# Kernel optimization log

Measured on AMD Instinct MI355X. Metric: run time of the kernel, lower is better.

## Reference

```python
import jax, jax.numpy as jnp
import numpy as np

N = 8192
NFEAT = 512
NHID = 256
NCLASS = 128


def setup_inputs() -> dict:
    key = jax.random.key(0)
    k1, k2, k3, k4 = jax.random.split(key, 4)
    feature_s = jax.random.normal(k1, (N, NFEAT), dtype=jnp.float32)
    feature_t = jax.random.normal(k2, (N, NFEAT), dtype=jnp.float32)
    # nn.Linear(in, out, bias=False) weight has shape [out, in]
    w1 = jax.random.normal(k3, (NHID, NFEAT), dtype=jnp.float32) * (1.0 / np.sqrt(NFEAT))
    w2 = jax.random.normal(k4, (NCLASS, NHID), dtype=jnp.float32) * (1.0 / np.sqrt(NHID))
    return {"feature_s": feature_s, "feature_t": feature_t, "w1": w1, "w2": w2}


def reference(feature_s, feature_t, w1, w2):
    # adj = softmax(feature_s @ feature_t^T) over rows (dim=1)
    adj = jax.nn.softmax(feature_s @ feature_t.T, axis=1)  # [N, N]
    # GCN layer 1: linear(adj @ x) with x = feature_s
    x1 = (adj @ feature_s) @ w1.T  # [N, NHID]
    # GCN layer 2
    x2 = (adj @ x1) @ w2.T  # [N, NCLASS]
    return (x1, x2)
```

## Files before the change

### kernel.cpp

```cpp
#include <hip/hip_runtime.h>
#include <stdint.h>


typedef unsigned short u16;
typedef short bf16x8 __attribute__((ext_vector_type(8)));
typedef _Float16 f16x8 __attribute__((ext_vector_type(8)));
typedef float f32x4 __attribute__((ext_vector_type(4)));

#define EPI_STOREB 0
#define EPI_PARTH  1

__device__ __forceinline__ u16 f2bf(float f) {
  unsigned u = __float_as_uint(f);
  u += 0x7fffu + ((u >> 16) & 1u);
  return (u16)(u >> 16);
}
__device__ __forceinline__ u16 f2h(float f) {
  union { _Float16 h; u16 u; } cv; cv.h = (_Float16)f; return cv.u;
}
__device__ __forceinline__ float h2f(u16 u) {
  union { u16 u; _Float16 h; } cv; cv.u = u; return (float)cv.h;
}
__device__ __forceinline__ int swz8(int r) { return (r ^ (r >> 3)) & 7; }
__device__ __forceinline__ int swz16(int r) { return (r ^ (r >> 4)) & 15; }

__device__ __forceinline__ void async16(const void* g, void* lds) {
  __builtin_amdgcn_global_load_lds(
      (const __attribute__((address_space(1))) unsigned int*)g,
      (__attribute__((address_space(3))) unsigned int*)lds, 16, 0, 0);
}

__global__ __launch_bounds__(256) void conv_probe(
    const float* __restrict__ Fs, const float* __restrict__ Ft,
    const float* __restrict__ W1, const float* __restrict__ W2,
    u16* __restrict__ Fsf, u16* __restrict__ Ftf,
    u16* __restrict__ W1f, u16* __restrict__ W2h,
    int* __restrict__ rmap, int* __restrict__ cmap) {
  const int bx = blockIdx.x, tid = threadIdx.x;
  if (bx < 4176) {
    const float* src; u16* dst; size_t i; bool tobf = false;
    if (bx < 2048)      { src = Fs; dst = Fsf; i = ((size_t)bx * 256 + tid) * 8; }
    else if (bx < 4096) { src = Ft; dst = Ftf; i = ((size_t)(bx - 2048) * 256 + tid) * 8; }
    else if (bx < 4160) { src = W1; dst = W1f; i = ((size_t)(bx - 4096) * 256 + tid) * 8; }
    else                { src = W2; dst = W2h; i = ((size_t)(bx - 4160) * 256 + tid) * 8; tobf = true; }
    const float4 a = *(const float4*)(src + i);
    const float4 b = *(const float4*)(src + i + 4);
    bf16x8 o;
    if (tobf) {
      o[0] = (short)f2bf(a.x); o[1] = (short)f2bf(a.y); o[2] = (short)f2bf(a.z); o[3] = (short)f2bf(a.w);
      o[4] = (short)f2bf(b.x); o[5] = (short)f2bf(b.y); o[6] = (short)f2bf(b.z); o[7] = (short)f2bf(b.w);
    } else {
      o[0] = (short)f2h(a.x); o[1] = (short)f2h(a.y); o[2] = (short)f2h(a.z); o[3] = (short)f2h(a.w);
      o[4] = (short)f2h(b.x); o[5] = (short)f2h(b.y); o[6] = (short)f2h(b.z); o[7] = (short)f2h(b.w);
    }
    *(bf16x8*)(dst + i) = o;
    return;
  }
  if (tid >= 64) return;
  const int lane = tid & 63;
  const int t = lane & 15, quad = lane >> 4;
  bf16x8 avt, av1;
  const u16 bt = f2bf((float)t), b1 = 0x3f80;
#pragma unroll
  for (int j = 0; j < 8; ++j) { ((u16*)&avt)[j] = bt; ((u16*)&av1)[j] = b1; }
  f32x4 z = {0.f, 0.f, 0.f, 0.f};
  f32x4 r1 = __builtin_amdgcn_mfma_f32_16x16x32_bf16(avt, av1, z, 0, 0, 0);
  f32x4 r2 = __builtin_amdgcn_mfma_f32_16x16x32_bf16(av1, avt, z, 0, 0, 0);
#pragma unroll
  for (int e = 0; e < 4; ++e) {
    int r = (int)(r1[e] * 0.03125f + 0.5f);
    int c = (int)(r2[e] * 0.03125f + 0.5f);
    if (r < 0 || r > 15) r = quad * 4 + e;
    if (c < 0 || c > 15) c = t;
    rmap[lane * 4 + e] = r;
    cmap[lane * 4 + e] = c;
  }
}

__global__ __launch_bounds__(512) void gemm_pexp_f16_256(
    const u16* __restrict__ A, const u16* __restrict__ B, int K, int N,
    u16* __restrict__ P, float* __restrict__ rsp,
    const int* __restrict__ rmap, const int* __restrict__ cmap) {
  __shared__ __align__(16) u16 lA[256 * 64];
  __shared__ __align__(16) u16 lB[128 * 64];
  __shared__ float lrs[256][2];

  const int tid = threadIdx.x;
  const int wave = tid >> 6, lane = tid & 63;
  const int quad = lane >> 4, t = lane & 15;
  const int bm = blockIdx.y * 256, bn = blockIdx.x * 128;
  const int wm = (wave & 3) * 64, wn = (wave >> 2) * 64;

  f32x4 acc[4][4];
#pragma unroll
  for (int i = 0; i < 4; ++i)
#pragma unroll
    for (int j = 0; j < 4; ++j) acc[i][j] = (f32x4){0.f, 0.f, 0.f, 0.f};

  const int srow = tid >> 3, schk = tid & 7;
  const u16* pA[4]; const u16* pB[2];
#pragma unroll
  for (int j = 0; j < 4; ++j) {
    const int r = j * 64 + srow;
    pA[j] = A + (size_t)(bm + r) * K + (schk ^ swz8(r)) * 8;
  }
#pragma unroll
  for (int j = 0; j < 2; ++j) {
    const int r = j * 64 + srow;
    pB[j] = B + (size_t)(bn + r) * K + (schk ^ swz8(r)) * 8;
  }

  int aoffx[4], boffx[4];
#pragma unroll
  for (int i = 0; i < 4; ++i) {
    const int rm = wm + i * 16 + t;
    aoffx[i] = rm * 128 + (swz8(rm) << 4);
    const int rn = wn + i * 16 + t;
    boffx[i] = rn * 128 + (swz8(rn) << 4);
  }
  const int sq0 = quad << 4, sq1 = (quad << 4) | 64;

  for (int k0 = 0; k0 < K; k0 += 64) {
#pragma unroll
    for (int j = 0; j < 4; ++j) {
      async16(pA[j], (char*)lA + j * 8192 + wave * 1024);
      pA[j] += 64;
    }
#pragma unroll
    for (int j = 0; j < 2; ++j) {
      async16(pB[j], (char*)lB + j * 8192 + wave * 1024);
      pB[j] += 64;
    }
    __syncthreads();
#pragma unroll
    for (int s = 0; s < 2; ++s) {
      const int sq = s ? sq1 : sq0;
      f16x8 av[4], bv[4];
#pragma unroll
      for (int i = 0; i < 4; ++i) {
        av[i] = *(const f16x8*)((const char*)lA + (aoffx[i] ^ sq));
        bv[i] = *(const f16x8*)((const char*)lB + (boffx[i] ^ sq));
      }
#pragma unroll
      for (int mi = 0; mi < 4; ++mi)
#pragma unroll
        for (int ni = 0; ni < 4; ++ni)
          acc[mi][ni] = __builtin_amdgcn_mfma_f32_16x16x32_f16(av[mi], bv[ni], acc[mi][ni], 0, 0, 0);
    }
    __syncthreads();
  }

  int rl[4], cl[4];
#pragma unroll
  for (int e = 0; e < 4; ++e) {
    rl[e] = rmap[lane * 4 + e];
    cl[e] = cmap[lane * 4 + e];
  }
#pragma unroll
  for (int mi = 0; mi < 4; ++mi)
#pragma unroll
    for (int e = 0; e < 4; ++e) {
      const int rloc = wm + mi * 16 + rl[e];
      const int row = bm + rloc;
      float s = 0.f;
#pragma unroll
      for (int ni = 0; ni < 4; ++ni) {
        float p = __expf(acc[mi][ni][e] - 100.0f);
        s += p;
        P[(size_t)row * N + (bn + wn + ni * 16 + cl[e])] = f2bf(p);
      }
      s += __shfl_xor(s, 1, 64);
      s += __shfl_xor(s, 2, 64);
      s += __shfl_xor(s, 4, 64);
      s += __shfl_xor(s, 8, 64);
      if (t == 0) lrs[rloc][wave >> 2] = s;
    }
  __syncthreads();
  if (tid < 256)
    rsp[(size_t)blockIdx.x * 8192 + bm + tid] = lrs[tid][0] + lrs[tid][1];
}

__global__ __launch_bounds__(256) void finalize_invl(
    const float* __restrict__ rsp, float* __restrict__ invl) {
  const int row = blockIdx.x * 256 + threadIdx.x;
  float s = 0.f;
#pragma unroll 8
  for (int b = 0; b < 64; ++b) s += rsp[(size_t)b * 8192 + row];
  invl[row] = 1.0f / s;
}

template <int EPI, int F16>
__global__ __launch_bounds__(256) void gemm_nt(
    const u16* __restrict__ A, const u16* __restrict__ B, int K, int Kc, int N,
    u16* __restrict__ outp, const float* __restrict__ invl,
    const int* __restrict__ rmap, const int* __restrict__ cmap) {
  __shared__ __align__(16) u16 lA[128 * 64];
  __shared__ __align__(16) u16 lB[128 * 64];

  const int tid = threadIdx.x;
  const int wave = tid >> 6, lane = tid & 63;
  const int quad = lane >> 4, t = lane & 15;
  const int bm = blockIdx.y * 128, bn = blockIdx.x * 128;
  const int wm = (wave & 1) * 64, wn = (wave >> 1) * 64;
  const int koff = blockIdx.z * Kc;

  f32x4 acc[4][4];
#pragma unroll
  for (int i = 0; i < 4; ++i)
#pragma unroll
    for (int j = 0; j < 4; ++j) acc[i][j] = (f32x4){0.f, 0.f, 0.f, 0.f};

  const int srow = tid >> 3, schk = tid & 7;
  const u16* pA[4]; const u16* pB[4];
#pragma unroll
  for (int j = 0; j < 4; ++j) {
    const int r = j * 32 + srow;
    const int c = schk ^ swz8(r);
    pA[j] = A + (size_t)(bm + r) * K + koff + c * 8;
    pB[j] = B + (size_t)(bn + r) * K + koff + c * 8;
  }

  int aoffx[4], boffx[4];
#pragma unroll
  for (int i = 0; i < 4; ++i) {
    const int rm = wm + i * 16 + t;
    aoffx[i] = rm * 128 + (swz8(rm) << 4);
    const int rn = wn + i * 16 + t;
    boffx[i] = rn * 128 + (swz8(rn) << 4);
  }
  const int sq0 = quad << 4, sq1 = (quad << 4) | 64;

  for (int k0 = 0; k0 < Kc; k0 += 64) {
#pragma unroll
    for (int j = 0; j < 4; ++j) {
      async16(pA[j], (char*)lA + j * 4096 + wave * 1024);
      async16(pB[j], (char*)lB + j * 4096 + wave * 1024);
      pA[j] += 64; pB[j] += 64;
    }
    __syncthreads();
#pragma unroll
    for (int s = 0; s < 2; ++s) {
      const int sq = s ? sq1 : sq0;
      bf16x8 av[4], bv[4];
#pragma unroll
      for (int i = 0; i < 4; ++i) {
        av[i] = *(const bf16x8*)((const char*)lA + (aoffx[i] ^ sq));
        bv[i] = *(const bf16x8*)((const char*)lB + (boffx[i] ^ sq));
      }
#pragma unroll
      for (int mi = 0; mi < 4; ++mi)
#pragma unroll
        for (int ni = 0; ni < 4; ++ni) {
          if constexpr (F16)
            acc[mi][ni] = __builtin_amdgcn_mfma_f32_16x16x32_f16(
                __builtin_bit_cast(f16x8, av[mi]), __builtin_bit_cast(f16x8, bv[ni]),
                acc[mi][ni], 0, 0, 0);
          else
            acc[mi][ni] = __builtin_amdgcn_mfma_f32_16x16x32_bf16(av[mi], bv[ni], acc[mi][ni], 0, 0, 0);
        }
    }
    __syncthreads();
  }

  int rl[4], cl[4];
#pragma unroll
  for (int e = 0; e < 4; ++e) {
    rl[e] = rmap[lane * 4 + e];
    cl[e] = cmap[lane * 4 + e];
  }
  const size_t zoff = (size_t)blockIdx.z * ((size_t)gridDim.y * 128) * N;
#pragma unroll
  for (int mi = 0; mi < 4; ++mi)
#pragma unroll
    for (int e = 0; e < 4; ++e) {
      const int row = bm + wm + mi * 16 + rl[e];
      const float sc = (EPI == EPI_PARTH) ? invl[row] : 1.0f;
#pragma unroll
      for (int ni = 0; ni < 4; ++ni) {
        const size_t idx = (size_t)row * N + (bn + wn + ni * 16 + cl[e]);
        if (EPI == EPI_PARTH) outp[zoff + idx] = f2h(acc[mi][ni][e] * sc);
        else                  outp[idx] = f2bf(acc[mi][ni][e]);
      }
    }
}

__global__ __launch_bounds__(256) void gemm_nt128(
    const u16* __restrict__ A, const u16* __restrict__ B, int K, int Kc, int N,
    u16* __restrict__ outp, const float* __restrict__ invl,
    const int* __restrict__ rmap, const int* __restrict__ cmap) {
  __shared__ __align__(16) u16 lA[128 * 128];
  __shared__ __align__(16) u16 lB[128 * 128];

  const int tid = threadIdx.x;
  const int wave = tid >> 6, lane = tid & 63;
  const int quad = lane >> 4, t = lane & 15;
  const int bm = blockIdx.y * 128, bn = blockIdx.x * 128;
  const int wm = (wave & 1) * 64, wn = (wave >> 1) * 64;
  const int koff = blockIdx.z * Kc;

  f32x4 acc[4][4];
#pragma unroll
  for (int i = 0; i < 4; ++i)
#pragma unroll
    for (int j = 0; j < 4; ++j) acc[i][j] = (f32x4){0.f, 0.f, 0.f, 0.f};

  const int srow = tid >> 4, schk = tid & 15;
  const u16* pA[8]; const u16* pB[8];
#pragma unroll
  for (int j = 0; j < 8; ++j) {
    const int r = j * 16 + srow;
    const int c = schk ^ swz16(r);
    pA[j] = A + (size_t)(bm + r) * K + koff + c * 8;
    pB[j] = B + (size_t)(bn + r) * K + koff + c * 8;
  }

  int aoffx[4], boffx[4];
#pragma unroll
  for (int i = 0; i < 4; ++i) {
    const int rm = wm + i * 16 + t;
    aoffx[i] = rm * 256 + (swz16(rm) << 4);
    const int rn = wn + i * 16 + t;
    boffx[i] = rn * 256 + (swz16(rn) << 4);
  }

  for (int k0 = 0; k0 < Kc; k0 += 128) {
#pragma unroll
    for (int j = 0; j < 8; ++j) {
      async16(pA[j], (char*)lA + j * 4096 + tid * 16);
      async16(pB[j], (char*)lB + j * 4096 + tid * 16);
      pA[j] += 128; pB[j] += 128;
    }
    __syncthreads();
#pragma unroll
    for (int s = 0; s < 4; ++s) {
      const int sq = (s << 6) | (quad << 4);
      bf16x8 av[4], bv[4];
#pragma unroll
      for (int i = 0; i < 4; ++i) {
        av[i] = *(const bf16x8*)((const char*)lA + (aoffx[i] ^ sq));
        bv[i] = *(const bf16x8*)((const char*)lB + (boffx[i] ^ sq));
      }
#pragma unroll
      for (int mi = 0; mi < 4; ++mi)
#pragma unroll
        for (int ni = 0; ni < 4; ++ni)
          acc[mi][ni] = __builtin_amdgcn_mfma_f32_16x16x32_bf16(av[mi], bv[ni], acc[mi][ni], 0, 0, 0);
    }
    __syncthreads();
  }

  int rl[4], cl[4];
#pragma unroll
  for (int e = 0; e < 4; ++e) {
    rl[e] = rmap[lane * 4 + e];
    cl[e] = cmap[lane * 4 + e];
  }
  const size_t zoff = (size_t)blockIdx.z * ((size_t)gridDim.y * 128) * N;
#pragma unroll
  for (int mi = 0; mi < 4; ++mi)
#pragma unroll
    for (int e = 0; e < 4; ++e) {
      const int row = bm + wm + mi * 16 + rl[e];
      const float sc = invl[row];
#pragma unroll
      for (int ni = 0; ni < 4; ++ni) {
        const size_t idx = (size_t)row * N + (bn + wn + ni * 16 + cl[e]);
        outp[zoff + idx] = f2h(acc[mi][ni][e] * sc);
      }
    }
}

__global__ __launch_bounds__(512) void gemm_ntw128(
    const u16* __restrict__ A, const u16* __restrict__ B, int K, int Kc, int N,
    u16* __restrict__ outp, const float* __restrict__ invl,
    const int* __restrict__ rmap, const int* __restrict__ cmap) {
  __shared__ __align__(16) u16 lA[128 * 128];
  __shared__ __align__(16) u16 lB[256 * 128];

  const int tid = threadIdx.x;
  const int wave = tid >> 6, lane = tid & 63;
  const int quad = lane >> 4, t = lane & 15;
  const int bm = blockIdx.y * 128, bn = blockIdx.x * 256;
  const int wm = (wave >> 2) * 64, wn = (wave & 3) * 64;
  const int koff = blockIdx.z * Kc;

  f32x4 acc[4][4];
#pragma unroll
  for (int i = 0; i < 4; ++i)
#pragma unroll
    for (int j = 0; j < 4; ++j) acc[i][j] = (f32x4){0.f, 0.f, 0.f, 0.f};

  const int srow = tid >> 4, schk = tid & 15;
  const u16* pA[4]; const u16* pB[8];
#pragma unroll
  for (int j = 0; j < 4; ++j) {
    const int r = j * 32 + srow;
    pA[j] = A + (size_t)(bm + r) * K + koff + (schk ^ swz16(r)) * 8;
  }
#pragma unroll
  for (int j = 0; j < 8; ++j) {
    const int r = j * 32 + srow;
    pB[j] = B + (size_t)(bn + r) * K + koff + (schk ^ swz16(r)) * 8;
  }

  int aoffx[4], boffx[4];
#pragma unroll
  for (int i = 0; i < 4; ++i) {
    const int rm = wm + i * 16 + t;
    aoffx[i] = rm * 256 + (swz16(rm) << 4);
    const int rn = wn + i * 16 + t;
    boffx[i] = rn * 256 + (swz16(rn) << 4);
  }

  for (int k0 = 0; k0 < Kc; k0 += 128) {
#pragma unroll
    for (int j = 0; j < 4; ++j) {
      async16(pA[j], (char*)lA + j * 8192 + tid * 16);
      pA[j] += 128;
    }
#pragma unroll
    for (int j = 0; j < 8; ++j) {
      async16(pB[j], (char*)lB + j * 8192 + tid * 16);
      pB[j] += 128;
    }
    __syncthreads();
#pragma unroll
    for (int s = 0; s < 4; ++s) {
      const int sq = (s << 6) | (quad << 4);
      bf16x8 av[4], bv[4];
#pragma unroll
      for (int i = 0; i < 4; ++i) {
        av[i] = *(const bf16x8*)((const char*)lA + (aoffx[i] ^ sq));
        bv[i] = *(const bf16x8*)((const char*)lB + (boffx[i] ^ sq));
      }
#pragma unroll
      for (int mi = 0; mi < 4; ++mi)
#pragma unroll
        for (int ni = 0; ni < 4; ++ni)
          acc[mi][ni] = __builtin_amdgcn_mfma_f32_16x16x32_bf16(av[mi], bv[ni], acc[mi][ni], 0, 0, 0);
    }
    __syncthreads();
  }

  int rl[4], cl[4];
#pragma unroll
  for (int e = 0; e < 4; ++e) {
    rl[e] = rmap[lane * 4 + e];
    cl[e] = cmap[lane * 4 + e];
  }
  const size_t zoff = (size_t)blockIdx.z * ((size_t)gridDim.y * 128) * N;
#pragma unroll
  for (int mi = 0; mi < 4; ++mi)
#pragma unroll
    for (int e = 0; e < 4; ++e) {
      const int row = bm + wm + mi * 16 + rl[e];
      const float sc = invl[row];
#pragma unroll
      for (int ni = 0; ni < 4; ++ni) {
        const size_t idx = (size_t)row * N + (bn + wn + ni * 16 + cl[e]);
        outp[zoff + idx] = f2h(acc[mi][ni][e] * sc);
      }
    }
}

__global__ __launch_bounds__(256) void combine1(
    const u16* __restrict__ pp, const float* __restrict__ invl,
    float* __restrict__ x1f, u16* __restrict__ x1h) {
  const size_t i = ((size_t)blockIdx.x * 256 + threadIdx.x) * 8;
  const bf16x8 p0 = *(const bf16x8*)(pp + i);
  const bf16x8 p1 = *(const bf16x8*)(pp + 2097152 + i);
  const bf16x8 p2 = *(const bf16x8*)(pp + 4194304 + i);
  const bf16x8 p3 = *(const bf16x8*)(pp + 6291456 + i);
  float4 o0, o1;
  bf16x8 oh;
#pragma unroll
  for (int j = 0; j < 8; ++j) {
    const float v = h2f((u16)p0[j]) + h2f((u16)p1[j]) + h2f((u16)p2[j]) + h2f((u16)p3[j]);
    if (j < 4) ((float*)&o0)[j] = v; else ((float*)&o1)[j - 4] = v;
    oh[j] = (short)f2bf(v);
  }
  *(float4*)(x1f + i) = o0;
  *(float4*)(x1f + i + 4) = o1;
  *(bf16x8*)(x1h + i) = oh;
}

__global__ __launch_bounds__(256) void combine2(
    const u16* __restrict__ pp, const float* __restrict__ invl,
    float* __restrict__ x2f) {
  const size_t i = ((size_t)blockIdx.x * 256 + threadIdx.x) * 8;
  float v[8] = {0.f, 0.f, 0.f, 0.f, 0.f, 0.f, 0.f, 0.f};
#pragma unroll
  for (int z = 0; z < 8; ++z) {
    const bf16x8 p = *(const bf16x8*)(pp + (size_t)z * 1048576 + i);
#pragma unroll
    for (int j = 0; j < 8; ++j) v[j] += h2f((u16)p[j]);
  }
  float4 o0, o1;
#pragma unroll
  for (int j = 0; j < 4; ++j) { ((float*)&o0)[j] = v[j]; ((float*)&o1)[j] = v[j + 4]; }
  *(float4*)(x2f + i) = o0;
  *(float4*)(x2f + i + 4) = o1;
}

extern "C" void kernel_launch(void* const* d_in, const int* in_sizes, int n_in,
                              void* d_out, int out_size, void* d_ws, size_t ws_size,
                              hipStream_t stream) {
  const float* Fs = (const float*)d_in[0];
  const float* Ft = (const float*)d_in[1];
  const float* W1 = (const float*)d_in[2];
  const float* W2 = (const float*)d_in[3];

  char* ws = (char*)d_ws;
  u16*   P    = (u16*)(ws);
  u16*   Fsf  = (u16*)(ws + 134217728);
  u16*   Ftf  = (u16*)(ws + 142606336);
  u16*   pp   = (u16*)(ws + 134217728);
  float* rsp  = (float*)(ws + 150994944);
  u16*   Y1T  = (u16*)(ws + 153092096);
  u16*   x1h  = (u16*)(ws + 157286400);
  u16*   Y2T  = (u16*)(ws + 161480704);
  float* invl = (float*)(ws + 163577856);
  int*   rmap = (int*)  (ws + 163610624);
  int*   cmap = (int*)  (ws + 163611648);
  u16*   W1f  = (u16*)(ws + 163612672);
  u16*   W2h  = (u16*)(ws + 163874816);

  float* x1f = (float*)d_out;
  float* x2f = (float*)d_out + 2097152;

  dim3 blk(256);
  conv_probe<<<4177, blk, 0, stream>>>(Fs, Ft, W1, W2, Fsf, Ftf, W1f, W2h, rmap, cmap);
  gemm_pexp_f16_256<<<dim3(64, 32), dim3(512), 0, stream>>>(
      Fsf, Ftf, 512, 8192, P, rsp, rmap, cmap);
  finalize_invl<<<32, blk, 0, stream>>>(rsp, invl);
  gemm_nt<EPI_STOREB, 1><<<dim3(64, 2), blk, 0, stream>>>(
      W1f, Fsf, 512, 512, 8192, Y1T, nullptr, rmap, cmap);
  gemm_ntw128<<<dim3(1, 64, 4), dim3(512), 0, stream>>>(
      P, Y1T, 8192, 2048, 256, pp, invl, rmap, cmap);
  combine1<<<1024, blk, 0, stream>>>(pp, invl, x1f, x1h);
  gemm_nt<EPI_STOREB, 0><<<dim3(64, 1), blk, 0, stream>>>(
      W2h, x1h, 256, 256, 8192, Y2T, nullptr, rmap, cmap);
  gemm_nt128<<<dim3(1, 64, 8), blk, 0, stream>>>(
      P, Y2T, 8192, 1024, 128, pp, invl, rmap, cmap);
  combine2<<<512, blk, 0, stream>>>(pp, invl, x2f);
}
```

Measured before the change: 276.8 us.

## Fuse invl finalize into GEMMs and combine1 with second-layer Y2T GEMM

Removes the finalize_invl kernel by having each split-K GEMM block sum its 128 rows' partial row-sums into shared memory. Merges combine1 and the small W2 GEMM into one kernel that reduces the split-K partials, writes x1 in fp32, and keeps the bf16 x1 tile in LDS to compute Y2T directly. This removes three launches and the x1h round trip through global memory. The cost is that every split-K block now repeats the 64-way row-sum reduction, and the fused kernel runs only 64 blocks.

New measurement: 279.3 us. Within noise of the previous version (+0.9%).

```diff
diff --git a/kernel.cpp b/kernel.cpp
--- a/kernel.cpp
+++ b/kernel.cpp
@@ -180,15 +180,6 @@
     rsp[(size_t)blockIdx.x * 8192 + bm + tid] = lrs[tid][0] + lrs[tid][1];
 }
 
-__global__ __launch_bounds__(256) void finalize_invl(
-    const float* __restrict__ rsp, float* __restrict__ invl) {
-  const int row = blockIdx.x * 256 + threadIdx.x;
-  float s = 0.f;
-#pragma unroll 8
-  for (int b = 0; b < 64; ++b) s += rsp[(size_t)b * 8192 + row];
-  invl[row] = 1.0f / s;
-}
-
 template <int EPI, int F16>
 __global__ __launch_bounds__(256) void gemm_nt(
     const u16* __restrict__ A, const u16* __restrict__ B, int K, int Kc, int N,
@@ -286,10 +277,11 @@
 
 __global__ __launch_bounds__(256) void gemm_nt128(
     const u16* __restrict__ A, const u16* __restrict__ B, int K, int Kc, int N,
-    u16* __restrict__ outp, const float* __restrict__ invl,
+    u16* __restrict__ outp, const float* __restrict__ rsp,
     const int* __restrict__ rmap, const int* __restrict__ cmap) {
   __shared__ __align__(16) u16 lA[128 * 128];
   __shared__ __align__(16) u16 lB[128 * 128];
+  __shared__ float linvl[128];
 
   const int tid = threadIdx.x;
   const int wave = tid >> 6, lane = tid & 63;
@@ -298,6 +290,14 @@
   const int wm = (wave & 1) * 64, wn = (wave >> 1) * 64;
   const int koff = blockIdx.z * Kc;
 
+  if (tid < 128) {
+    const int row = bm + tid;
+    float s = 0.f;
+#pragma unroll 8
+    for (int b = 0; b < 64; ++b) s += rsp[(size_t)b * 8192 + row];
+    linvl[tid] = 1.0f / s;
+  }
+
   f32x4 acc[4][4];
 #pragma unroll
   for (int i = 0; i < 4; ++i)
@@ -360,8 +360,9 @@
   for (int mi = 0; mi < 4; ++mi)
 #pragma unroll
     for (int e = 0; e < 4; ++e) {
-      const int row = bm + wm + mi * 16 + rl[e];
-      const float sc = invl[row];
+      const int rloc = wm + mi * 16 + rl[e];
+      const int row = bm + rloc;
+      const float sc = linvl[rloc];
 #pragma unroll
       for (int ni = 0; ni < 4; ++ni) {
         const size_t idx = (size_t)row * N + (bn + wn + ni * 16 + cl[e]);
@@ -372,10 +373,11 @@
 
 __global__ __launch_bounds__(512) void gemm_ntw128(
     const u16* __restrict__ A, const u16* __restrict__ B, int K, int Kc, int N,
-    u16* __restrict__ outp, const float* __restrict__ invl,
+    u16* __restrict__ outp, const float* __restrict__ rsp,
     const int* __restrict__ rmap, const int* __restrict__ cmap) {
   __shared__ __align__(16) u16 lA[128 * 128];
   __shared__ __align__(16) u16 lB[256 * 128];
+  __shared__ float linvl[128];
 
   const int tid = threadIdx.x;
   const int wave = tid >> 6, lane = tid & 63;
@@ -384,6 +386,14 @@
   const int wm = (wave >> 2) * 64, wn = (wave & 3) * 64;
   const int koff = blockIdx.z * Kc;
 
+  if (tid < 128) {
+    const int row = bm + tid;
+    float s = 0.f;
+#pragma unroll 8
+    for (int b = 0; b < 64; ++b) s += rsp[(size_t)b * 8192 + row];
+    linvl[tid] = 1.0f / s;
+  }
+
   f32x4 acc[4][4];
 #pragma unroll
   for (int i = 0; i < 4; ++i)
@@ -453,8 +463,9 @@
   for (int mi = 0; mi < 4; ++mi)
 #pragma unroll
     for (int e = 0; e < 4; ++e) {
-      const int row = bm + wm + mi * 16 + rl[e];
-      const float sc = invl[row];
+      const int rloc = wm + mi * 16 + rl[e];
+      const int row = bm + rloc;
+      const float sc = linvl[rloc];
 #pragma unroll
       for (int ni = 0; ni < 4; ++ni) {
         const size_t idx = (size_t)row * N + (bn + wn + ni * 16 + cl[e]);
@@ -463,25 +474,111 @@
     }
 }
 
-__global__ __launch_bounds__(256) void combine1(
-    const u16* __restrict__ pp, const float* __restrict__ invl,
-    float* __restrict__ x1f, u16* __restrict__ x1h) {
-  const size_t i = ((size_t)blockIdx.x * 256 + threadIdx.x) * 8;
-  const bf16x8 p0 = *(const bf16x8*)(pp + i);
-  const bf16x8 p1 = *(const bf16x8*)(pp + 2097152 + i);
-  const bf16x8 p2 = *(const bf16x8*)(pp + 4194304 + i);
-  const bf16x8 p3 = *(const bf16x8*)(pp + 6291456 + i);
-  float4 o0, o1;
-  bf16x8 oh;
-#pragma unroll
-  for (int j = 0; j < 8; ++j) {
-    const float v = h2f((u16)p0[j]) + h2f((u16)p1[j]) + h2f((u16)p2[j]) + h2f((u16)p3[j]);
-    if (j < 4) ((float*)&o0)[j] = v; else ((float*)&o1)[j - 4] = v;
-    oh[j] = (short)f2bf(v);
-  }
-  *(float4*)(x1f + i) = o0;
-  *(float4*)(x1f + i + 4) = o1;
-  *(bf16x8*)(x1h + i) = oh;
+__global__ __launch_bounds__(256) void c1gy2(
+    const u16* __restrict__ pp, const u16* __restrict__ W2h,
+    float* __restrict__ x1f, u16* __restrict__ Y2T,
+    const int* __restrict__ rmap, const int* __restrict__ cmap) {
+  __shared__ __align__(16) u16 x1l[4][128][64];
+  __shared__ __align__(16) u16 lA[128 * 64];
+
+  const int tid = threadIdx.x;
+  const int g = blockIdx.x;
+
+#pragma unroll
+  for (int it = 0; it < 16; ++it) {
+    const int f = (it * 256 + tid) * 8;
+    const int r = f >> 8, c = f & 255;
+    const size_t i = (size_t)(g * 128 + r) * 256 + c;
+    const bf16x8 p0 = *(const bf16x8*)(pp + i);
+    const bf16x8 p1 = *(const bf16x8*)(pp + 2097152 + i);
+    const bf16x8 p2 = *(const bf16x8*)(pp + 4194304 + i);
+    const bf16x8 p3 = *(const bf16x8*)(pp + 6291456 + i);
+    float4 o0, o1;
+    bf16x8 oh;
+#pragma unroll
+    for (int j = 0; j < 8; ++j) {
+      const float v = h2f((u16)p0[j]) + h2f((u16)p1[j]) + h2f((u16)p2[j]) + h2f((u16)p3[j]);
+      if (j < 4) ((float*)&o0)[j] = v; else ((float*)&o1)[j - 4] = v;
+      oh[j] = (short)f2bf(v);
+    }
+    *(float4*)(x1f + i) = o0;
+    *(float4*)(x1f + i + 4) = o1;
+    const int kt = c >> 6, ch = (c & 63) >> 3;
+    *(bf16x8*)((char*)&x1l[kt][r][0] + ((ch ^ swz8(r)) << 4)) = oh;
+  }
+  __syncthreads();
+
+  const int wave = tid >> 6, lane = tid & 63;
+  const int quad = lane >> 4, t = lane & 15;
+  const int wm = (wave & 1) * 64, wn = (wave >> 1) * 64;
+  const int bn = g * 128;
+
+  f32x4 acc[4][4];
+#pragma unroll
+  for (int i = 0; i < 4; ++i)
+#pragma unroll
+    for (int j = 0; j < 4; ++j) acc[i][j] = (f32x4){0.f, 0.f, 0.f, 0.f};
+
+  const int srow = tid >> 3, schk = tid & 7;
+  const u16* pA[4];
+#pragma unroll
+  for (int j = 0; j < 4; ++j) {
+    const int r = j * 32 + srow;
+    pA[j] = W2h + (size_t)r * 256 + (schk ^ swz8(r)) * 8;
+  }
+
+  int aoffx[4], boffx[4];
+#pragma unroll
+  for (int i = 0; i < 4; ++i) {
+    const int rm = wm + i * 16 + t;
+    aoffx[i] = rm * 128 + (swz8(rm) << 4);
+    const int rn = wn + i * 16 + t;
+    boffx[i] = rn * 128 + (swz8(rn) << 4);
+  }
+  const int sq0 = quad << 4, sq1 = (quad << 4) | 64;
+
+  for (int kt = 0; kt < 4; ++kt) {
+#pragma unroll
+    for (int j = 0; j < 4; ++j) {
+      async16(pA[j], (char*)lA + j * 4096 + wave * 1024);
+      pA[j] += 64;
+    }
+    __syncthreads();
+#pragma unroll
+    for (int s = 0; s < 2; ++s) {
+      const int sq = s ? sq1 : sq0;
+      bf16x8 av[4], bv[4];
+#pragma unroll
+      for (int i = 0; i < 4; ++i) {
+        av[i] = *(const bf16x8*)((const char*)lA + (aoffx[i] ^ sq));
+        bv[i] = *(const bf16x8*)((const char*)&x1l[kt][0][0] + (boffx[i] ^ sq));
+      }
+#pragma unroll
+      for (int mi = 0; mi < 4; ++mi)
+#pragma unroll
+        for (int ni = 0; ni < 4; ++ni)
+          acc[mi][ni] = __builtin_amdgcn_mfma_f32_16x16x32_bf16(av[mi], bv[ni], acc[mi][ni], 0, 0, 0);
+    }
+    __syncthreads();
+  }
+
+  int rl[4], cl[4];
+#pragma unroll
+  for (int e = 0; e < 4; ++e) {
+    rl[e] = rmap[lane * 4 + e];
+    cl[e] = cmap[lane * 4 + e];
+  }
+#pragma unroll
+  for (int mi = 0; mi < 4; ++mi)
+#pragma unroll
+    for (int e = 0; e < 4; ++e) {
+      const int row = wm + mi * 16 + rl[e];
+#pragma unroll
+      for (int ni = 0; ni < 4; ++ni) {
+        const size_t idx = (size_t)row * 8192 + (bn + wn + ni * 16 + cl[e]);
+        Y2T[idx] = f2bf(acc[mi][ni][e]);
+      }
+    }
 }
 
 __global__ __launch_bounds__(256) void combine2(
@@ -517,9 +614,7 @@
   u16*   pp   = (u16*)(ws + 134217728);
   float* rsp  = (float*)(ws + 150994944);
   u16*   Y1T  = (u16*)(ws + 153092096);
-  u16*   x1h  = (u16*)(ws + 157286400);
   u16*   Y2T  = (u16*)(ws + 161480704);
-  float* invl = (float*)(ws + 163577856);
   int*   rmap = (int*)  (ws + 163610624);
   int*   cmap = (int*)  (ws + 163611648);
   u16*   W1f  = (u16*)(ws + 163612672);
@@ -532,15 +627,12 @@
   conv_probe<<<4177, blk, 0, stream>>>(Fs, Ft, W1, W2, Fsf, Ftf, W1f, W2h, rmap, cmap);
   gemm_pexp_f16_256<<<dim3(64, 32), dim3(512), 0, stream>>>(
       Fsf, Ftf, 512, 8192, P, rsp, rmap, cmap);
-  finalize_invl<<<32, blk, 0, stream>>>(rsp, invl);
   gemm_nt<EPI_STOREB, 1><<<dim3(64, 2), blk, 0, stream>>>(
       W1f, Fsf, 512, 512, 8192, Y1T, nullptr, rmap, cmap);
   gemm_ntw128<<<dim3(1, 64, 4), dim3(512), 0, stream>>>(
-      P, Y1T, 8192, 2048, 256, pp, invl, rmap, cmap);
-  combine1<<<1024, blk, 0, stream>>>(pp, invl, x1f, x1h);
-  gemm_nt<EPI_STOREB, 0><<<dim3(64, 1), blk, 0, stream>>>(
-      W2h, x1h, 256, 256, 8192, Y2T, nullptr, rmap, cmap);
+      P, Y1T, 8192, 2048, 256, pp, rsp, rmap, cmap);
+  c1gy2<<<64, blk, 0, stream>>>(pp, W2h, x1f, Y2T, rmap, cmap);
   gemm_nt128<<<dim3(1, 64, 8), blk, 0, stream>>>(
-      P, Y2T, 8192, 1024, 128, pp, invl, rmap, cmap);
-  combine2<<<512, blk, 0, stream>>>(pp, invl, x2f);
-}
+      P, Y2T, 8192, 1024, 128, pp, rsp, rmap, cmap);
+  combine2<<<512, blk, 0, stream>>>(pp, nullptr, x2f);
+}
```
